# Performance work log

Measured on AMD Instinct MI355X. Metric: run time of the kernel, lower is better.

Reference implementation:

```python
import jax, jax.numpy as jnp
import numpy as np

D_MODEL = 16   # output feature dim of channel_proj
D_STATE = 8
D_CONV = 2
D_INNER = 4    # expand * inner mamba d_model (2*2)
DT_RANK = 1    # ceil(2/16)
NUM_PAIRS = 36
B, W, T = 8, 8, 1024


def setup_inputs() -> dict:
    key = jax.random.key(0)
    ks = jax.random.split(key, 12)
    s = 0.5
    return {
        "raw_signals": jax.random.normal(ks[0], (B, W, NUM_PAIRS, 2, T), jnp.float32),
        "in_proj_w": jax.random.normal(ks[1], (2 * D_INNER, 2), jnp.float32) * s,
        "conv_w": jax.random.normal(ks[2], (D_INNER, D_CONV), jnp.float32) * s,
        "conv_b": jax.random.normal(ks[3], (D_INNER,), jnp.float32) * 0.1,
        "x_proj_w": jax.random.normal(ks[4], (DT_RANK + 2 * D_STATE, D_INNER), jnp.float32) * s,
        "dt_proj_w": jax.random.normal(ks[5], (D_INNER, DT_RANK), jnp.float32) * s,
        "dt_proj_b": jax.random.normal(ks[6], (D_INNER,), jnp.float32) * 0.1,
        # S4D-real init: A_log = log(arange(1..d_state)) per inner channel
        "A_log": jnp.log(jnp.broadcast_to(jnp.arange(1, D_STATE + 1, dtype=jnp.float32), (D_INNER, D_STATE))),
        "D_skip": jnp.ones((D_INNER,), jnp.float32),
        "out_proj_w": jax.random.normal(ks[7], (2, D_INNER), jnp.float32) * s,
        "proj_w": jax.random.normal(ks[8], (D_MODEL, 2), jnp.float32) * s,
        "proj_b": jax.random.normal(ks[9], (D_MODEL,), jnp.float32) * 0.1,
    }


def _mamba_forward(x_in, in_proj_w, conv_w, conv_b, x_proj_w, dt_proj_w,
                   dt_proj_b, A_log, D_skip, out_proj_w):
    # x_in: (N, T, 2)
    N, Tlen, _ = x_in.shape
    xz = jnp.einsum('ntc,dc->ntd', x_in, in_proj_w)          # (N,T,2*d_inner)
    x, z = jnp.split(xz, 2, axis=-1)                          # (N,T,d_inner) each
    # causal depthwise conv1d, kernel size D_CONV
    xp = jnp.pad(x, ((0, 0), (D_CONV - 1, 0), (0, 0)))
    x = sum(xp[:, k:k + Tlen] * conv_w[:, k] for k in range(D_CONV)) + conv_b
    x = jax.nn.silu(x)
    # input-dependent dt, B, C
    x_dbl = jnp.einsum('ntd,ed->nte', x, x_proj_w)            # (N,T,dt_rank+2*d_state)
    dt, Bm, Cm = jnp.split(x_dbl, [DT_RANK, DT_RANK + D_STATE], axis=-1)
    dt = jax.nn.softplus(jnp.einsum('ntr,dr->ntd', dt, dt_proj_w) + dt_proj_b)
    A = -jnp.exp(A_log)                                       # (d_inner,d_state)
    deltaA = jnp.exp(dt[..., None] * A)                       # (N,T,d_inner,d_state)
    deltaBx = dt[..., None] * Bm[:, :, None, :] * x[..., None]

    def step(h, inputs):
        dA_t, dBx_t, c_t = inputs
        h = dA_t * h + dBx_t                                  # (N,d_inner,d_state)
        y_t = jnp.einsum('nds,ns->nd', h, c_t)
        return h, y_t

    h0 = jnp.zeros((N, D_INNER, D_STATE), x.dtype)
    _, ys = jax.lax.scan(
        step, h0,
        (deltaA.transpose(1, 0, 2, 3), deltaBx.transpose(1, 0, 2, 3), Cm.transpose(1, 0, 2)))
    y = ys.transpose(1, 0, 2) + x * D_skip                    # (N,T,d_inner)
    y = y * jax.nn.silu(z)
    return jnp.einsum('ntd,cd->ntc', y, out_proj_w)           # (N,T,2)


def reference(raw_signals, in_proj_w, conv_w, conv_b, x_proj_w, dt_proj_w,
              dt_proj_b, A_log, D_skip, out_proj_w, proj_w, proj_b):
    Bsz, Wn, P, C, Tlen = raw_signals.shape
    # per-window loop in torch does identical math -> flatten windows into batch
    x_in = raw_signals.transpose(0, 1, 2, 4, 3).reshape(-1, Tlen, C)  # (B*W*P, T, 2)
    out = _mamba_forward(x_in, in_proj_w, conv_w, conv_b, x_proj_w, dt_proj_w,
                         dt_proj_b, A_log, D_skip, out_proj_w)
    feat = out.mean(axis=1)                                   # (B*W*P, 2)
    proj = jax.nn.relu(feat @ proj_w.T + proj_b)              # dropout is eval no-op
    proj = proj.reshape(Bsz, Wn, P, -1)                       # (B,W,P,d_model)
    return proj.mean(axis=2)                                  # (B,W,d_model)
```

## Files before the change

### kernel.cpp

```cpp
#include <hip/hip_runtime.h>
#include <hip/hip_fp16.h>


typedef float v2f __attribute__((ext_vector_type(2)));

#define TT 1024
#define TC 32
#define NSEGS 16
#define SEGLEN (TT / NSEGS)
#define NCHUNK (SEGLEN / TC)
#define NUM_PAIRS 36
#define NSEQ 2304

#define DT_OFF 0
#define DS_OFF 128
#define BC_OFF 256
#define BC_STRIDE 33
#define PER_HALF_STRIDE 528
#define PER_WAVE (2 * PER_HALF_STRIDE)
#define STAGE_TOTAL (8 * PER_WAVE)

__device__ __forceinline__ float fast_silu(float v) {
    float e = __builtin_amdgcn_exp2f(v * -1.4426950408889634f);
    return v * __builtin_amdgcn_rcpf(1.0f + e);
}
__device__ __forceinline__ float fast_softplus(float v) {
    float e = __builtin_amdgcn_exp2f(v * 1.4426950408889634f);
    return __builtin_amdgcn_logf(1.0f + e) * 0.6931471805599453f;
}
__device__ __forceinline__ uint pk_h2(float a, float b) {
    return __builtin_bit_cast(uint, __builtin_amdgcn_cvt_pkrtz(a, b));
}

__global__ __launch_bounds__(512, 4)
void pm_kernel(const float* __restrict__ raw,
               const float* __restrict__ in_proj_w,
               const float* __restrict__ conv_w,
               const float* __restrict__ conv_b,
               const float* __restrict__ x_proj_w,
               const float* __restrict__ dt_proj_w,
               const float* __restrict__ dt_proj_b,
               const float* __restrict__ A_log,
               const float* __restrict__ D_skip,
               const float* __restrict__ out_proj_w,
               const float* __restrict__ proj_w,
               const float* __restrict__ proj_b,
               float* __restrict__ out)
{
    __shared__ float lds[STAGE_TOTAL];

    const int tid  = threadIdx.x;
    const int wid  = tid >> 6;
    const int lane = tid & 63;
    const int half = lane >> 5;
    const int lh   = lane & 31;
    const int g    = wid * 2 + half;
    const int n    = blockIdx.x;
    const float* rp = raw + (size_t)n * (2 * TT);

    float* hb = lds + wid * PER_WAVE + half * PER_HALF_STRIDE;

    float ip0[8], ip1[8];
#pragma unroll
    for (int j = 0; j < 8; ++j) { ip0[j] = in_proj_w[2*j]; ip1[j] = in_proj_w[2*j+1]; }
    float dpw[4], dpb[4], Dsk[4], ow0[4], ow1[4], xp0[4];
    v2f alp[2], bep[2], gap[2], dep[2], cbp[2], zc0[2], zc1[2];
#pragma unroll
    for (int d = 0; d < 4; ++d) {
        dpw[d] = dt_proj_w[d]; dpb[d] = dt_proj_b[d];
        Dsk[d] = D_skip[d]; ow0[d] = out_proj_w[d]; ow1[d] = out_proj_w[4+d];
        xp0[d] = x_proj_w[d];
    }
#pragma unroll
    for (int k = 0; k < 2; ++k) {
        int d0 = 2*k, d1 = 2*k + 1;
        float cw00 = conv_w[2*d0], cw01 = conv_w[2*d0+1];
        float cw10 = conv_w[2*d1], cw11 = conv_w[2*d1+1];
        alp[k] = (v2f){cw00*ip0[d0], cw10*ip0[d1]};
        bep[k] = (v2f){cw00*ip1[d0], cw10*ip1[d1]};
        gap[k] = (v2f){cw01*ip0[d0], cw11*ip0[d1]};
        dep[k] = (v2f){cw01*ip1[d0], cw11*ip1[d1]};
        cbp[k] = (v2f){conv_b[d0], conv_b[d1]};
        zc0[k] = (v2f){ip0[4+d0], ip0[4+d1]};
        zc1[k] = (v2f){ip1[4+d0], ip1[4+d1]};
    }
    v2f xbc[8][4];
#pragma unroll
    for (int s = 0; s < 8; ++s)
#pragma unroll
        for (int d = 0; d < 4; ++d)
            xbc[s][d] = (v2f){x_proj_w[4*(1+s) + d], x_proj_w[4*(9+s) + d]};

    const float LOG2E = 1.4426950408889634f;
    const int   d_idx = lh >> 3;
    const int   s_idx = lh & 7;
    const float A2ds  = -__expf(A_log[lh]) * LOG2E;
    const float owd0  = out_proj_w[d_idx];
    const float owd1  = out_proj_w[4 + d_idx];

    const float* dtp = hb + DT_OFF + d_idx;
    const uint*  dsp = (const uint*)(hb + DS_OFF) + d_idx;
    const uint*  bcp = (const uint*)(hb + BC_OFF) + s_idx * BC_STRIDE;

    float A_run = 1.0f, hB = 0.0f, W = 0.0f, S = 0.0f;
    float sacc0 = 0.f, sacc1 = 0.f;

    const int seg0 = g * SEGLEN;

    int t0 = seg0 + lh;
    float c0  = rp[t0];
    float c1  = rp[TT + t0];
    float c0m = (t0 > 0) ? rp[t0 - 1]      : 0.0f;
    float c1m = (t0 > 0) ? rp[TT + t0 - 1] : 0.0f;

    for (int chunk = 0; chunk < NCHUNK; ++chunk) {
        float p0 = 0.f, p1 = 0.f, p0m = 0.f, p1m = 0.f;
        if (chunk + 1 < NCHUNK) {
            int tn = seg0 + (chunk + 1) * TC + lh;
            p0  = rp[tn];       p1  = rp[TT + tn];
            p0m = rp[tn - 1];   p1m = rp[TT + tn - 1];
        }

        float x[4], sz[4];
        const v2f c0v = {c0, c0}, c1v = {c1, c1};
        const v2f c0mv = {c0m, c0m}, c1mv = {c1m, c1m};
#pragma unroll
        for (int k = 0; k < 2; ++k) {
            v2f v = __builtin_elementwise_fma(alp[k], c0mv,
                    __builtin_elementwise_fma(bep[k], c1mv,
                    __builtin_elementwise_fma(gap[k], c0v,
                    __builtin_elementwise_fma(dep[k], c1v, cbp[k]))));
            v2f zv = __builtin_elementwise_fma(zc0[k], c0v, zc1[k] * c1v);
            x[2*k]    = fast_silu(v.x);
            x[2*k+1]  = fast_silu(v.y);
            sz[2*k]   = fast_silu(zv.x);
            sz[2*k+1] = fast_silu(zv.y);
        }

        float dtin = xp0[0]*x[0] + xp0[1]*x[1] + xp0[2]*x[2] + xp0[3]*x[3];

        v2f bc[8];
#pragma unroll
        for (int s = 0; s < 8; ++s) {
            v2f a = xbc[s][0] * (v2f){x[0], x[0]};
            a = __builtin_elementwise_fma(xbc[s][1], (v2f){x[1], x[1]}, a);
            a = __builtin_elementwise_fma(xbc[s][2], (v2f){x[2], x[2]}, a);
            bc[s] = __builtin_elementwise_fma(xbc[s][3], (v2f){x[3], x[3]}, a);
        }

        float dt[4];
#pragma unroll
        for (int d = 0; d < 4; ++d) {
            dt[d] = fast_softplus(dtin*dpw[d] + dpb[d]);
            float g2 = x[d] * Dsk[d] * sz[d];
            sacc0 = fmaf(g2, ow0[d], sacc0);
            sacc1 = fmaf(g2, ow1[d], sacc1);
        }

        *(float4*)(hb + DT_OFF + lh*4) = make_float4(dt[0], dt[1], dt[2], dt[3]);
        *(uint4*)((uint*)(hb + DS_OFF) + lh*4) =
            make_uint4(pk_h2(dt[0]*x[0], sz[0]), pk_h2(dt[1]*x[1], sz[1]),
                       pk_h2(dt[2]*x[2], sz[2]), pk_h2(dt[3]*x[3], sz[3]));
        uint* bcw = (uint*)(hb + BC_OFF) + lh;
#pragma unroll
        for (int s = 0; s < 8; ++s)
            bcw[s * BC_STRIDE] = pk_h2(bc[s].x, bc[s].y);

#pragma unroll
        for (int t2 = 0; t2 < TC; ++t2) {
            float dtv = dtp[t2*4];
            uint  uds = dsp[t2*4];
            uint  ubc = bcp[t2];
            __half2 prod = __hmul2(__builtin_bit_cast(__half2, uds),
                                   __builtin_bit_cast(__half2, ubc));
            float b = __half2float(__low2half(prod));
            float q = __half2float(__high2half(prod));
            float a = __builtin_amdgcn_exp2f(dtv * A2ds);
            A_run *= a;
            hB = fmaf(a, hB, b);
            W  = fmaf(A_run, q, W);
            S  = fmaf(hB, q, S);
        }

        c0 = p0; c1 = p1; c0m = p0m; c1m = p1m;
    }

    __syncthreads();
    float2* comb = (float2*)lds;
    comb[g*32 + lh] = make_float2(A_run, hB);
    __syncthreads();

    float h_in = 0.0f;
#pragma unroll
    for (int gg = 0; gg < NSEGS - 1; ++gg) {
        if (gg < g) {
            float2 abg = comb[gg*32 + lh];
            h_in = fmaf(abg.x, h_in, abg.y);
        }
    }

    float F = fmaf(h_in, W, S);
    float tot0 = fmaf(F, owd0, sacc0);
    float tot1 = fmaf(F, owd1, sacc1);
#pragma unroll
    for (int m = 16; m >= 1; m >>= 1) {
        tot0 += __shfl_xor(tot0, m, 64);
        tot1 += __shfl_xor(tot1, m, 64);
    }
    float* part = lds + 1024;
    if (lh == 0) {
        part[g*2]     = tot0;
        part[g*2 + 1] = tot1;
    }
    __syncthreads();

    if (tid < 16) {
        float f0 = 0.f, f1 = 0.f;
#pragma unroll
        for (int gg = 0; gg < NSEGS; ++gg) {
            f0 += part[gg*2];
            f1 += part[gg*2 + 1];
        }
        f0 *= (1.0f / (float)TT);
        f1 *= (1.0f / (float)TT);
        float pv = f0*proj_w[2*tid] + f1*proj_w[2*tid + 1] + proj_b[tid];
        pv = fmaxf(pv, 0.0f);
        atomicAdd(out + (n / NUM_PAIRS) * 16 + tid, pv * (1.0f / NUM_PAIRS));
    }
}

extern "C" void kernel_launch(void* const* d_in, const int* in_sizes, int n_in,
                              void* d_out, int out_size, void* d_ws, size_t ws_size,
                              hipStream_t stream)
{
    const float* raw        = (const float*)d_in[0];
    const float* in_proj_w  = (const float*)d_in[1];
    const float* conv_w     = (const float*)d_in[2];
    const float* conv_b     = (const float*)d_in[3];
    const float* x_proj_w   = (const float*)d_in[4];
    const float* dt_proj_w  = (const float*)d_in[5];
    const float* dt_proj_b  = (const float*)d_in[6];
    const float* A_log      = (const float*)d_in[7];
    const float* D_skip     = (const float*)d_in[8];
    const float* out_proj_w = (const float*)d_in[9];
    const float* proj_w     = (const float*)d_in[10];
    const float* proj_b     = (const float*)d_in[11];

    hipMemsetAsync(d_out, 0, (size_t)out_size * sizeof(float), stream);

    pm_kernel<<<dim3(NSEQ), dim3(512), 0, stream>>>(
        raw, in_proj_w, conv_w, conv_b, x_proj_w, dt_proj_w, dt_proj_b,
        A_log, D_skip, out_proj_w, proj_w, proj_b, (float*)d_out);
}
```

Before: 122.8 us.

## Split scan into per-segment kernel and separate cross-segment combine kernel

Cuts each sequence into 8 segments instead of 16 and assigns half-waves to (sequence, segment) pairs across 256-thread blocks. The in-block LDS exchange of segment carries and the barriers are replaced by writes to a global workspace, followed by a second kernel that chains the segment carries and does the projection and atomic accumulation. The per-step recurrence is rewritten with packed two-wide FMAs. The intent is to remove block-wide syncs and the serial combine from the scan kernel and to raise occupancy, at the cost of a second launch, workspace traffic and longer per-segment serial chains.

After: 119.8 us. -2.4%, faster.

```diff
diff --git a/kernel.cpp b/kernel.cpp
--- a/kernel.cpp
+++ b/kernel.cpp
@@ -6,11 +6,12 @@
 
 #define TT 1024
 #define TC 32
-#define NSEGS 16
+#define NSEGS 8
 #define SEGLEN (TT / NSEGS)
 #define NCHUNK (SEGLEN / TC)
 #define NUM_PAIRS 36
 #define NSEQ 2304
+#define NHALF (NSEQ * NSEGS)
 
 #define DT_OFF 0
 #define DS_OFF 128
@@ -18,7 +19,7 @@
 #define BC_STRIDE 33
 #define PER_HALF_STRIDE 528
 #define PER_WAVE (2 * PER_HALF_STRIDE)
-#define STAGE_TOTAL (8 * PER_WAVE)
+#define STAGE_TOTAL (4 * PER_WAVE)
 
 __device__ __forceinline__ float fast_silu(float v) {
     float e = __builtin_amdgcn_exp2f(v * -1.4426950408889634f);
@@ -32,20 +33,19 @@
     return __builtin_bit_cast(uint, __builtin_amdgcn_cvt_pkrtz(a, b));
 }
 
-__global__ __launch_bounds__(512, 4)
-void pm_kernel(const float* __restrict__ raw,
-               const float* __restrict__ in_proj_w,
-               const float* __restrict__ conv_w,
-               const float* __restrict__ conv_b,
-               const float* __restrict__ x_proj_w,
-               const float* __restrict__ dt_proj_w,
-               const float* __restrict__ dt_proj_b,
-               const float* __restrict__ A_log,
-               const float* __restrict__ D_skip,
-               const float* __restrict__ out_proj_w,
-               const float* __restrict__ proj_w,
-               const float* __restrict__ proj_b,
-               float* __restrict__ out)
+__global__ __launch_bounds__(256, 4)
+void pm_scan(const float* __restrict__ raw,
+             const float* __restrict__ in_proj_w,
+             const float* __restrict__ conv_w,
+             const float* __restrict__ conv_b,
+             const float* __restrict__ x_proj_w,
+             const float* __restrict__ dt_proj_w,
+             const float* __restrict__ dt_proj_b,
+             const float* __restrict__ A_log,
+             const float* __restrict__ D_skip,
+             const float* __restrict__ out_proj_w,
+             float4* __restrict__ wsA,
+             float2* __restrict__ wsS)
 {
     __shared__ float lds[STAGE_TOTAL];
 
@@ -54,8 +54,9 @@
     const int lane = tid & 63;
     const int half = lane >> 5;
     const int lh   = lane & 31;
-    const int g    = wid * 2 + half;
-    const int n    = blockIdx.x;
+    const int H    = (blockIdx.x * 4 + wid) * 2 + half;
+    const int n    = H >> 3;
+    const int g    = H & 7;
     const float* rp = raw + (size_t)n * (2 * TT);
 
     float* hb = lds + wid * PER_WAVE + half * PER_HALF_STRIDE;
@@ -95,14 +96,13 @@
     const int   d_idx = lh >> 3;
     const int   s_idx = lh & 7;
     const float A2ds  = -__expf(A_log[lh]) * LOG2E;
-    const float owd0  = out_proj_w[d_idx];
-    const float owd1  = out_proj_w[4 + d_idx];
 
     const float* dtp = hb + DT_OFF + d_idx;
     const uint*  dsp = (const uint*)(hb + DS_OFF) + d_idx;
     const uint*  bcp = (const uint*)(hb + BC_OFF) + s_idx * BC_STRIDE;
 
-    float A_run = 1.0f, hB = 0.0f, W = 0.0f, S = 0.0f;
+    v2f AhB = {1.0f, 0.0f};
+    v2f WS  = {0.0f, 0.0f};
     float sacc0 = 0.f, sacc1 = 0.f;
 
     const int seg0 = g * SEGLEN;
@@ -176,56 +176,69 @@
             float b = __half2float(__low2half(prod));
             float q = __half2float(__high2half(prod));
             float a = __builtin_amdgcn_exp2f(dtv * A2ds);
-            A_run *= a;
-            hB = fmaf(a, hB, b);
-            W  = fmaf(A_run, q, W);
-            S  = fmaf(hB, q, S);
+            AhB = __builtin_elementwise_fma((v2f){a, a}, AhB, (v2f){0.0f, b});
+            WS  = __builtin_elementwise_fma(AhB, (v2f){q, q}, WS);
         }
 
         c0 = p0; c1 = p1; c0m = p0m; c1m = p1m;
     }
 
-    __syncthreads();
-    float2* comb = (float2*)lds;
-    comb[g*32 + lh] = make_float2(A_run, hB);
-    __syncthreads();
-
-    float h_in = 0.0f;
-#pragma unroll
-    for (int gg = 0; gg < NSEGS - 1; ++gg) {
-        if (gg < g) {
-            float2 abg = comb[gg*32 + lh];
-            h_in = fmaf(abg.x, h_in, abg.y);
-        }
-    }
-
-    float F = fmaf(h_in, W, S);
-    float tot0 = fmaf(F, owd0, sacc0);
-    float tot1 = fmaf(F, owd1, sacc1);
+    float s0 = sacc0, s1 = sacc1;
+#pragma unroll
+    for (int m = 16; m >= 1; m >>= 1) {
+        s0 += __shfl_xor(s0, m, 64);
+        s1 += __shfl_xor(s1, m, 64);
+    }
+    wsA[(size_t)H * 32 + lh] = make_float4(AhB.x, AhB.y, WS.x, WS.y);
+    if (lh == 0) wsS[H] = make_float2(s0, s1);
+}
+
+__global__ __launch_bounds__(256, 4)
+void pm_comb(const float4* __restrict__ wsA,
+             const float2* __restrict__ wsS,
+             const float* __restrict__ out_proj_w,
+             const float* __restrict__ proj_w,
+             const float* __restrict__ proj_b,
+             float* __restrict__ out)
+{
+    const int tid  = threadIdx.x;
+    const int wid  = tid >> 6;
+    const int lane = tid & 63;
+    const int half = lane >> 5;
+    const int lh   = lane & 31;
+    const int n    = blockIdx.x * 8 + wid * 2 + half;
+
+    const int   d_idx = lh >> 3;
+    const float owd0  = out_proj_w[d_idx];
+    const float owd1  = out_proj_w[4 + d_idx];
+
+    float h_in = 0.0f, F = 0.0f;
+#pragma unroll
+    for (int g = 0; g < NSEGS; ++g) {
+        float4 v = wsA[(size_t)(n * NSEGS + g) * 32 + lh];
+        F    = F + fmaf(h_in, v.z, v.w);
+        h_in = fmaf(v.x, h_in, v.y);
+    }
+
+    float tot0 = F * owd0;
+    float tot1 = F * owd1;
+    if (lh < NSEGS) {
+        float2 sc = wsS[n * NSEGS + lh];
+        tot0 += sc.x;
+        tot1 += sc.y;
+    }
 #pragma unroll
     for (int m = 16; m >= 1; m >>= 1) {
         tot0 += __shfl_xor(tot0, m, 64);
         tot1 += __shfl_xor(tot1, m, 64);
     }
-    float* part = lds + 1024;
-    if (lh == 0) {
-        part[g*2]     = tot0;
-        part[g*2 + 1] = tot1;
-    }
-    __syncthreads();
-
-    if (tid < 16) {
-        float f0 = 0.f, f1 = 0.f;
-#pragma unroll
-        for (int gg = 0; gg < NSEGS; ++gg) {
-            f0 += part[gg*2];
-            f1 += part[gg*2 + 1];
-        }
-        f0 *= (1.0f / (float)TT);
-        f1 *= (1.0f / (float)TT);
-        float pv = f0*proj_w[2*tid] + f1*proj_w[2*tid + 1] + proj_b[tid];
+
+    if (lh < 16) {
+        float f0 = tot0 * (1.0f / (float)TT);
+        float f1 = tot1 * (1.0f / (float)TT);
+        float pv = f0*proj_w[2*lh] + f1*proj_w[2*lh + 1] + proj_b[lh];
         pv = fmaxf(pv, 0.0f);
-        atomicAdd(out + (n / NUM_PAIRS) * 16 + tid, pv * (1.0f / NUM_PAIRS));
+        atomicAdd(out + (n / NUM_PAIRS) * 16 + lh, pv * (1.0f / NUM_PAIRS));
     }
 }
 
@@ -246,9 +259,15 @@
     const float* proj_w     = (const float*)d_in[10];
     const float* proj_b     = (const float*)d_in[11];
 
+    float4* wsA = (float4*)d_ws;
+    float2* wsS = (float2*)((char*)d_ws + (size_t)NHALF * 32 * 16);
+
     hipMemsetAsync(d_out, 0, (size_t)out_size * sizeof(float), stream);
 
-    pm_kernel<<<dim3(NSEQ), dim3(512), 0, stream>>>(
+    pm_scan<<<dim3(NSEQ), dim3(256), 0, stream>>>(
         raw, in_proj_w, conv_w, conv_b, x_proj_w, dt_proj_w, dt_proj_b,
-        A_log, D_skip, out_proj_w, proj_w, proj_b, (float*)d_out);
-}
+        A_log, D_skip, out_proj_w, wsA, wsS);
+
+    pm_comb<<<dim3(NSEQ / 8), dim3(256), 0, stream>>>(
+        wsA, wsS, out_proj_w, proj_w, proj_b, (float*)d_out);
+}
```
